# Optimization experiments

Measured on AMD Instinct MI355X. Metric: run time of the kernel, lower is better.

## Reference

```python
import jax, jax.numpy as jnp
import numpy as np

# Dims: batch=2, seqlen=L=384, d_inner=d=384, d_state=s=384, dt_rank=r=384, d_conv=4.
# NOTE: the original torch module only runs when L == d_inner == d_state == dt_rank
# (see its broadcasting in SelectiveScan and the Linear layer plumbing); we reproduce
# that exact (quirky) broadcast faithfully.
B_, L_, D_, S_, R_, K_ = 2, 384, 384, 384, 384, 4


def setup_inputs() -> dict:
    key = jax.random.key(0)
    ks = jax.random.split(key, 9)
    f32 = jnp.float32
    return {
        "x": jax.random.normal(ks[0], (B_, L_, D_), f32),
        "A_log": jax.random.normal(ks[1], (D_, S_), f32) * 0.02,
        "D": jax.random.normal(ks[2], (D_,), f32) * 0.02,
        "dt_w": jax.random.normal(ks[3], (D_, R_), f32) * 0.02,
        "dt_b": jax.random.normal(ks[4], (D_,), f32) * 0.02,
        "B_w": jax.random.normal(ks[5], (S_, D_), f32) * (1.0 / np.sqrt(D_)),
        "C_w": jax.random.normal(ks[6], (S_, D_), f32) * (1.0 / np.sqrt(D_)),
        "conv_w": jax.random.normal(ks[7], (D_, 1, K_), f32) * (1.0 / np.sqrt(K_)),
        "conv_b": jnp.zeros((D_,), f32),
    }


def _forward(x, A_log, D, dt_w, dt_b, B_w, C_w, conv_w, conv_b):
    b, L, d = x.shape
    A = -jnp.exp(A_log)                       # (d, s)
    dt = jax.nn.softplus(x @ dt_w.T + dt_b)   # (b, L, d)
    x_dbl = x @ B_w.T                         # (b, L, s)
    Bm = x_dbl @ B_w.T                        # (b, L, s)  (module applies B_proj twice)
    Cm = x_dbl @ C_w.T                        # (b, L, s)
    # causal depthwise conv1d: pad (k-1) on the left == torch pad k-1 then [:, :, :L]
    xc = jax.lax.conv_general_dilated(
        x.transpose(0, 2, 1), conv_w, (1,), [(conv_w.shape[-1] - 1, 0)],
        feature_group_count=d, dimension_numbers=("NCH", "OIH", "NCH"))
    xc = xc + conv_b[None, :, None]
    u = jax.nn.silu(xc.transpose(0, 2, 1))    # (b, L, d)
    # selective scan (faithful to the torch SelectiveScan broadcasting)
    deltaA = jnp.exp(dt[..., None] * A[None, None])          # (b, L, d, s)
    deltaB_u = dt[..., None] * Bm[:, None, :, :] * u[..., None]  # (b, L, d, s), needs L==d

    def step(h, inp):
        dA_i, dBu_i, C_i, u_i = inp
        h = dA_i * h + dBu_i                  # (b, d, s)
        y = jnp.sum(h * C_i[:, None, :], -1) + u_i * D  # (b, d)
        return h, y

    h0 = jnp.zeros((b, d, deltaA.shape[-1]), x.dtype)
    xs = (deltaA.transpose(1, 0, 2, 3), deltaB_u.transpose(1, 0, 2, 3),
          Cm.transpose(1, 0, 2), u.transpose(1, 0, 2))
    _, ys = jax.lax.scan(step, h0, xs)        # ys: (L, b, d)
    return ys.transpose(1, 0, 2)


def reference(x, A_log, D, dt_w, dt_b, B_w, C_w, conv_w, conv_b):
    return _forward(x, A_log, D, dt_w, dt_b, B_w, C_w, conv_w, conv_b)
```

## Files before the change

kernel.cpp:

```cpp
#include <hip/hip_runtime.h>
#include <math.h>

#define B_SZ 2
#define L_SZ 384
#define D_SZ 384
#define S_SZ 384
#define BLK_ELEMS (L_SZ * D_SZ)
#define TOT_ELEMS (B_SZ * L_SZ * D_SZ)
#define LOG2E 1.4426950408889634f

typedef __attribute__((ext_vector_type(8))) short bf16x8;
typedef __attribute__((ext_vector_type(4))) float f32x4;
typedef __attribute__((ext_vector_type(2))) unsigned int u32x2;

__device__ __forceinline__ float fexp2(float x) {
  return __builtin_amdgcn_exp2f(x);
}
__device__ __forceinline__ float softplus_f(float z) {
  return (z > 20.f) ? z : log1pf(__expf(z));
}
__device__ __forceinline__ unsigned short f2bf(float f) {
  unsigned int u = __float_as_uint(f);
  return (unsigned short)((u + 0x7FFFu + ((u >> 16) & 1u)) >> 16);
}
#define PIPELINE_FENCE() asm volatile("" ::: "memory")

template <int CTRL>
__device__ __forceinline__ float dpp_mov(float v) {
  return __int_as_float(
      __builtin_amdgcn_update_dpp(0, __float_as_int(v), CTRL, 0xF, 0xF, true));
}

__device__ __forceinline__ float fold_xor16(float r) {
#if __has_builtin(__builtin_amdgcn_permlane16_swap)
  const unsigned ru = __float_as_uint(r);
  u32x2 p = __builtin_amdgcn_permlane16_swap(ru, ru, false, false);
  return __uint_as_float(p[0]) + __uint_as_float(p[1]);
#else
  return r + __shfl_xor(r, 16, 64);
#endif
}
__device__ __forceinline__ float fold_xor32(float r) {
#if __has_builtin(__builtin_amdgcn_permlane32_swap)
  const unsigned ru = __float_as_uint(r);
  u32x2 p = __builtin_amdgcn_permlane32_swap(ru, ru, false, false);
  return __uint_as_float(p[0]) + __uint_as_float(p[1]);
#else
  return r + __shfl_xor(r, 32, 64);
#endif
}

__global__ __launch_bounds__(256) void cvt_bf16_kernel(
    const float* __restrict__ x, const float* __restrict__ dt_w,
    const float* __restrict__ B_w, const float* __restrict__ C_w,
    unsigned short* __restrict__ xbf, unsigned short* __restrict__ dtwbf,
    unsigned short* __restrict__ Bwbf, unsigned short* __restrict__ Cwbf) {
  const int blk = blockIdx.x;
  const float* src;
  unsigned short* dst;
  int base;
  if (blk < 288) { src = x; dst = xbf; base = blk; }
  else if (blk < 432) { src = dt_w; dst = dtwbf; base = blk - 288; }
  else if (blk < 576) { src = B_w; dst = Bwbf; base = blk - 432; }
  else { src = C_w; dst = Cwbf; base = blk - 576; }
  const int idx = base * 1024 + threadIdx.x * 4;
  const float4 v = *(const float4*)(src + idx);
  ushort4 o;
  o.x = f2bf(v.x); o.y = f2bf(v.y); o.z = f2bf(v.z); o.w = f2bf(v.w);
  *(ushort4*)(dst + idx) = o;
}

template <int MODE>
__global__ __launch_bounds__(128, 2) void mfma_dual_gemm(
    const unsigned short* __restrict__ Abf,
    const unsigned short* __restrict__ W1bf,
    const unsigned short* __restrict__ W2bf,
    const float* __restrict__ bias,
    float* __restrict__ O1, void* __restrict__ O2v) {
  __shared__ unsigned short sA[32 * 392];
  __shared__ unsigned short sW1[16 * 392];
  __shared__ unsigned short sW2[16 * 392];

  const int t = threadIdx.x;
  const int wv = t >> 6;
  const int lane = t & 63;
  const int nt = blockIdx.x;
  const int mrow = blockIdx.y;

  const unsigned short* Ab = Abf + mrow * 32 * 384;
  const unsigned short* W1b = W1bf + nt * 16 * 384;
  const unsigned short* W2b = W2bf + nt * 16 * 384;

#pragma unroll
  for (int it = 0; it < 12; ++it) {
    const int id = t + it * 128;
    const int row = id / 48, col = id - row * 48;
    *(bf16x8*)&sA[row * 392 + col * 8] = *(const bf16x8*)(Ab + id * 8);
  }
#pragma unroll
  for (int it = 0; it < 6; ++it) {
    const int id = t + it * 128;
    const int row = id / 48, col = id - row * 48;
    *(bf16x8*)&sW1[row * 392 + col * 8] = *(const bf16x8*)(W1b + id * 8);
    *(bf16x8*)&sW2[row * 392 + col * 8] = *(const bf16x8*)(W2b + id * 8);
  }
  __syncthreads();

  const int rc = lane & 15;
  const int quad = lane >> 4;
  bf16x8 af[12], w1f[12], w2f[12];
#pragma unroll
  for (int kt = 0; kt < 12; ++kt) {
    af[kt] = *(const bf16x8*)&sA[(wv * 16 + rc) * 392 + quad * 8 + kt * 32];
    w1f[kt] = *(const bf16x8*)&sW1[rc * 392 + quad * 8 + kt * 32];
    w2f[kt] = *(const bf16x8*)&sW2[rc * 392 + quad * 8 + kt * 32];
  }
  PIPELINE_FENCE();
  f32x4 acc1 = {0.f, 0.f, 0.f, 0.f};
  f32x4 acc2 = {0.f, 0.f, 0.f, 0.f};
#pragma unroll
  for (int kt = 0; kt < 12; ++kt) {
    acc1 = __builtin_amdgcn_mfma_f32_16x16x32_bf16(af[kt], w1f[kt], acc1, 0, 0, 0);
    acc2 = __builtin_amdgcn_mfma_f32_16x16x32_bf16(af[kt], w2f[kt], acc2, 0, 0, 0);
  }
  const int col = nt * 16 + rc;
  const int row0 = mrow * 32 + wv * 16 + quad * 4;
  if constexpr (MODE == 1) {
    unsigned short* O2 = (unsigned short*)O2v;
    const float bb = bias[col];
#pragma unroll
    for (int r = 0; r < 4; ++r) {
      O1[(row0 + r) * 384 + col] = softplus_f(acc1[r] + bb);
      O2[(row0 + r) * 384 + col] = f2bf(acc2[r]);
    }
  } else {
    float* O2 = (float*)O2v;
#pragma unroll
    for (int r = 0; r < 4; ++r) {
      O1[(row0 + r) * 384 + col] = acc1[r];
      O2[(row0 + r) * 384 + col] = acc2[r];
    }
  }
}

__global__ __launch_bounds__(256) void conv_tr_kernel(
    const float* __restrict__ x, const float* __restrict__ cw,
    const float* __restrict__ cb, const float* __restrict__ dt,
    float* __restrict__ u, float* __restrict__ dt_t,
    float* __restrict__ dtu_t) {
  __shared__ float Tdt[32][33];
  __shared__ float Tdu[32][33];
  const int tx = threadIdx.x;
  const int ty = threadIdx.y;
  const int b = blockIdx.z;
  const int i0 = blockIdx.y * 32;
  const int l0 = blockIdx.x * 32;
  const int gi = i0 + tx;
  const float cbv = cb[gi];
  const float cw0 = cw[gi * 4 + 0], cw1 = cw[gi * 4 + 1];
  const float cw2 = cw[gi * 4 + 2], cw3 = cw[gi * 4 + 3];
#pragma unroll
  for (int r = 0; r < 4; ++r) {
    const int l = l0 + ty + 8 * r;
    float acc = cbv;
    const float x3 = x[(b * L_SZ + l) * D_SZ + gi];
    const float x2 = (l >= 1) ? x[(b * L_SZ + l - 1) * D_SZ + gi] : 0.f;
    const float x1 = (l >= 2) ? x[(b * L_SZ + l - 2) * D_SZ + gi] : 0.f;
    const float x0 = (l >= 3) ? x[(b * L_SZ + l - 3) * D_SZ + gi] : 0.f;
    acc = fmaf(x0, cw0, acc);
    acc = fmaf(x1, cw1, acc);
    acc = fmaf(x2, cw2, acc);
    acc = fmaf(x3, cw3, acc);
    const float uv = acc / (1.f + __expf(-acc));
    const int off = (b * L_SZ + l) * D_SZ + gi;
    u[off] = uv;
    const float dtv = dt[off];
    Tdt[ty + 8 * r][tx] = dtv;
    Tdu[ty + 8 * r][tx] = dtv * uv;
  }
  __syncthreads();
#pragma unroll
  for (int r = 0; r < 4; ++r) {
    const int il = ty + 8 * r;
    const int off = (b * D_SZ + i0 + il) * L_SZ + l0 + tx;
    dt_t[off] = Tdt[tx][il];
    dtu_t[off] = Tdu[tx][il];
  }
}

struct ChunkS {
  f32x4 d0, d1, u0, u1;
  float c[8];
};

#define LOAD_CHUNK(K, B0, B1, B2, DTB, DUB)                                    \
  {                                                                            \
    asm volatile("global_load_dwordx4 %0, %1, off" : "=v"(K.d0) : "v"(DTB));   \
    asm volatile("global_load_dwordx4 %0, %1, off offset:16"                   \
                 : "=v"(K.d1) : "v"(DTB));                                     \
    asm volatile("global_load_dwordx4 %0, %1, off" : "=v"(K.u0) : "v"(DUB));   \
    asm volatile("global_load_dwordx4 %0, %1, off offset:16"                   \
                 : "=v"(K.u1) : "v"(DUB));                                     \
    asm volatile("global_load_dword %0, %1, off" : "=v"(K.c[0]) : "v"(B0));    \
    asm volatile("global_load_dword %0, %1, off offset:1536"                   \
                 : "=v"(K.c[1]) : "v"(B0));                                    \
    asm volatile("global_load_dword %0, %1, off offset:3072"                   \
                 : "=v"(K.c[2]) : "v"(B0));                                    \
    asm volatile("global_load_dword %0, %1, off" : "=v"(K.c[3]) : "v"(B1));    \
    asm volatile("global_load_dword %0, %1, off offset:1536"                   \
                 : "=v"(K.c[4]) : "v"(B1));                                    \
    asm volatile("global_load_dword %0, %1, off offset:3072"                   \
                 : "=v"(K.c[5]) : "v"(B1));                                    \
    asm volatile("global_load_dword %0, %1, off" : "=v"(K.c[6]) : "v"(B2));    \
    asm volatile("global_load_dword %0, %1, off offset:1536"                   \
                 : "=v"(K.c[7]) : "v"(B2));                                    \
  }

#define WAIT_CHUNK(K)                                                          \
  asm volatile("s_waitcnt vmcnt(24)"                                           \
               : "+v"(K.d0), "+v"(K.d1), "+v"(K.u0), "+v"(K.u1),               \
                 "+v"(K.c[0]), "+v"(K.c[1]), "+v"(K.c[2]), "+v"(K.c[3]),       \
                 "+v"(K.c[4]), "+v"(K.c[5]), "+v"(K.c[6]), "+v"(K.c[7]))

#define ADV_BASES()                                                            \
  { cb0 += 3072; cb1 += 3072; cb2 += 3072; dtB += 8; duB += 8; }

__global__ __launch_bounds__(384, 4) void scan_kernel(
    const float* __restrict__ A_log, const float* __restrict__ dt_t,
    const float* __restrict__ dtu_t, const float* __restrict__ Bm,
    const float* __restrict__ Cm, float* __restrict__ part) {
  const int bid = blockIdx.x;
  const int xcd = bid & 7;
  const int sid = xcd * 96 + (bid >> 3);
  const int w = threadIdx.x >> 6;
  const int lane = threadIdx.x & 63;
  const int b = sid / D_SZ;
  const int i = sid % D_SZ;
  const int j = w * 64 + lane;

  const float a2 = -__expf(A_log[i * S_SZ + j]) * LOG2E;
  const float bw = Bm[(b * D_SZ + i) * S_SZ + j];
  float h = 0.f;

  const float* dtB = dt_t + (b * D_SZ + i) * L_SZ;
  const float* duB = dtu_t + (b * D_SZ + i) * L_SZ;
  const float* cmrow = Cm + b * BLK_ELEMS + j;
  const float* cb0 = cmrow;
  const float* cb1 = cmrow + 3 * D_SZ;
  const float* cb2 = cmrow + 6 * D_SZ;

  const int sq = (((lane >> 3) & 1) << 2) | (((lane >> 2) & 1) << 1) | (lane & 1);
  const bool storer = (lane & 0x32) == 0;
  float* pstore = part + ((w * B_SZ + b) * D_SZ + i) * L_SZ + sq;

  asm volatile("" :: "v"(a2), "v"(bw));
  asm volatile("s_waitcnt vmcnt(0)");

  auto compute_chunk = [&](ChunkS& K) {
    float acc[8];
    const float dts[8] = {K.d0[0], K.d0[1], K.d0[2], K.d0[3],
                          K.d1[0], K.d1[1], K.d1[2], K.d1[3]};
    const float dus[8] = {K.u0[0], K.u0[1], K.u0[2], K.u0[3],
                          K.u1[0], K.u1[1], K.u1[2], K.u1[3]};
#pragma unroll
    for (int s = 0; s < 8; ++s) {
      const float e = fexp2(dts[s] * a2);
      h = fmaf(e, h, bw * dus[s]);
      acc[s] = h * K.c[s];
    }
    {
      const bool hi = (lane & 8) != 0;
#pragma unroll
      for (int q = 0; q < 4; ++q) {
        const float keep = hi ? acc[q + 4] : acc[q];
        const float send = hi ? acc[q] : acc[q + 4];
        acc[q] = keep + dpp_mov<0x140>(send);
      }
    }
    {
      const bool hi = (lane & 4) != 0;
#pragma unroll
      for (int q = 0; q < 2; ++q) {
        const float keep = hi ? acc[q + 2] : acc[q];
        const float send = hi ? acc[q] : acc[q + 2];
        acc[q] = keep + dpp_mov<0x141>(send);
      }
    }
    {
      const bool hi = (lane & 1) != 0;
      const float keep = hi ? acc[1] : acc[0];
      const float send = hi ? acc[0] : acc[1];
      acc[0] = keep + dpp_mov<0xB1>(send);
    }
    float r = acc[0];
    r += dpp_mov<0x4E>(r);
    r = fold_xor16(r);
    r = fold_xor32(r);
    if (storer) *pstore = r;
    pstore += 8;
  };

  ChunkS K0, K1, K2;
  LOAD_CHUNK(K0, cb0, cb1, cb2, dtB, duB);
  ADV_BASES();
  LOAD_CHUNK(K1, cb0, cb1, cb2, dtB, duB);
  ADV_BASES();
#pragma unroll 1
  for (int it = 0; it < 16; ++it) {
    LOAD_CHUNK(K2, cb0, cb1, cb2, dtB, duB);
    ADV_BASES();
    WAIT_CHUNK(K0);
    compute_chunk(K0);
    LOAD_CHUNK(K0, cb0, cb1, cb2, dtB, duB);
    ADV_BASES();
    WAIT_CHUNK(K1);
    compute_chunk(K1);
    LOAD_CHUNK(K1, cb0, cb1, cb2, dtB, duB);
    ADV_BASES();
    WAIT_CHUNK(K2);
    compute_chunk(K2);
  }
}

__global__ __launch_bounds__(256) void combine_kernel(
    const float* __restrict__ part, const float* __restrict__ u,
    const float* __restrict__ Dv, float* __restrict__ y) {
  __shared__ float T[32][33];
  const int tx = threadIdx.x;
  const int ty0 = threadIdx.y;
  const int b = blockIdx.z;
  const int i0 = blockIdx.y * 32;
  const int l0 = blockIdx.x * 32;
#pragma unroll
  for (int r = 0; r < 4; ++r) {
    const int il = ty0 + 8 * r;
    float s = 0.f;
#pragma unroll
    for (int w = 0; w < 6; ++w)
      s += part[((w * B_SZ + b) * D_SZ + i0 + il) * L_SZ + l0 + tx];
    T[il][tx] = s;
  }
  __syncthreads();
#pragma unroll
  for (int r = 0; r < 4; ++r) {
    const int ll = ty0 + 8 * r;
    const int gi = i0 + tx;
    const int off = (b * L_SZ + l0 + ll) * D_SZ + gi;
    y[off] = fmaf(u[off], Dv[gi], T[tx][ll]);
  }
}

extern "C" void kernel_launch(void* const* d_in, const int* in_sizes, int n_in,
                              void* d_out, int out_size, void* d_ws,
                              size_t ws_size, hipStream_t stream) {
  const float* x = (const float*)d_in[0];
  const float* A_log = (const float*)d_in[1];
  const float* D = (const float*)d_in[2];
  const float* dt_w = (const float*)d_in[3];
  const float* dt_b = (const float*)d_in[4];
  const float* B_w = (const float*)d_in[5];
  const float* C_w = (const float*)d_in[6];
  const float* conv_w = (const float*)d_in[7];
  const float* conv_b = (const float*)d_in[8];
  float* y = (float*)d_out;

  float* ws = (float*)d_ws;
  float* dt = ws;
  float* u = ws + TOT_ELEMS;
  float* Bm = ws + 2 * TOT_ELEMS;
  float* Cm = ws + 3 * TOT_ELEMS;
  float* dt_t = ws + 4 * TOT_ELEMS;
  float* dtu_t = ws + 5 * TOT_ELEMS;
  float* part = ws + 6 * TOT_ELEMS;
  unsigned short* bfarea = (unsigned short*)(ws + 12 * TOT_ELEMS);
  unsigned short* xbf = bfarea;
  unsigned short* dtwbf = bfarea + 294912;
  unsigned short* Bwbf = bfarea + 442368;
  unsigned short* Cwbf = bfarea + 589824;
  unsigned short* xdblbf = bfarea + 737280;

  cvt_bf16_kernel<<<720, 256, 0, stream>>>(x, dt_w, B_w, C_w, xbf, dtwbf, Bwbf, Cwbf);
  mfma_dual_gemm<1><<<dim3(24, 24), 128, 0, stream>>>(xbf, dtwbf, Bwbf, dt_b, dt, xdblbf);
  mfma_dual_gemm<2><<<dim3(24, 24), 128, 0, stream>>>(xdblbf, Bwbf, Cwbf, nullptr, Bm, Cm);
  conv_tr_kernel<<<dim3(L_SZ / 32, D_SZ / 32, B_SZ), dim3(32, 8), 0, stream>>>(
      x, conv_w, conv_b, dt, u, dt_t, dtu_t);
  scan_kernel<<<768, 384, 0, stream>>>(A_log, dt_t, dtu_t, Bm, Cm, part);
  combine_kernel<<<dim3(L_SZ / 32, D_SZ / 32, B_SZ), dim3(32, 8), 0, stream>>>(
      part, u, D, y);
}
```

Before: 139.7 us.

## Fuse bf16 conversion into GEMM loads, transpose Cm, split scan into wave blocks

Removes the separate fp32-to-bf16 conversion kernel: the GEMMs now load fp32 inputs and weights and convert them in-register with packed bf16 conversion instructions while filling LDS. The conv/transpose kernel additionally writes a transposed copy of Cm, so each scan lane can read contiguous dwordx4 vectors instead of eight strided scalar loads per chunk. The scan launch changes from 768 blocks of 384 threads to 4608 single-wave blocks. The trade-offs are an extra transpose write and read of Cm, and weights being converted redundantly in every GEMM block.

```diff
diff --git a/kernel.cpp b/kernel.cpp
--- a/kernel.cpp
+++ b/kernel.cpp
@@ -24,6 +24,17 @@
   return (unsigned short)((u + 0x7FFFu + ((u >> 16) & 1u)) >> 16);
 }
 #define PIPELINE_FENCE() asm volatile("" ::: "memory")
+
+__device__ __forceinline__ bf16x8 cvt8(const float* p) {
+  const f32x4 v0 = *(const f32x4*)p;
+  const f32x4 v1 = *(const f32x4*)(p + 4);
+  union { unsigned int u[4]; bf16x8 v; } r;
+  asm("v_cvt_pk_bf16_f32 %0, %1, %2" : "=v"(r.u[0]) : "v"(v0[0]), "v"(v0[1]));
+  asm("v_cvt_pk_bf16_f32 %0, %1, %2" : "=v"(r.u[1]) : "v"(v0[2]), "v"(v0[3]));
+  asm("v_cvt_pk_bf16_f32 %0, %1, %2" : "=v"(r.u[2]) : "v"(v1[0]), "v"(v1[1]));
+  asm("v_cvt_pk_bf16_f32 %0, %1, %2" : "=v"(r.u[3]) : "v"(v1[2]), "v"(v1[3]));
+  return r.v;
+}
 
 template <int CTRL>
 __device__ __forceinline__ float dpp_mov(float v) {
@@ -50,32 +61,10 @@
 #endif
 }
 
-__global__ __launch_bounds__(256) void cvt_bf16_kernel(
-    const float* __restrict__ x, const float* __restrict__ dt_w,
-    const float* __restrict__ B_w, const float* __restrict__ C_w,
-    unsigned short* __restrict__ xbf, unsigned short* __restrict__ dtwbf,
-    unsigned short* __restrict__ Bwbf, unsigned short* __restrict__ Cwbf) {
-  const int blk = blockIdx.x;
-  const float* src;
-  unsigned short* dst;
-  int base;
-  if (blk < 288) { src = x; dst = xbf; base = blk; }
-  else if (blk < 432) { src = dt_w; dst = dtwbf; base = blk - 288; }
-  else if (blk < 576) { src = B_w; dst = Bwbf; base = blk - 432; }
-  else { src = C_w; dst = Cwbf; base = blk - 576; }
-  const int idx = base * 1024 + threadIdx.x * 4;
-  const float4 v = *(const float4*)(src + idx);
-  ushort4 o;
-  o.x = f2bf(v.x); o.y = f2bf(v.y); o.z = f2bf(v.z); o.w = f2bf(v.w);
-  *(ushort4*)(dst + idx) = o;
-}
-
 template <int MODE>
 __global__ __launch_bounds__(128, 2) void mfma_dual_gemm(
-    const unsigned short* __restrict__ Abf,
-    const unsigned short* __restrict__ W1bf,
-    const unsigned short* __restrict__ W2bf,
-    const float* __restrict__ bias,
+    const void* __restrict__ Av, const float* __restrict__ W1,
+    const float* __restrict__ W2, const float* __restrict__ bias,
     float* __restrict__ O1, void* __restrict__ O2v) {
   __shared__ unsigned short sA[32 * 392];
   __shared__ unsigned short sW1[16 * 392];
@@ -87,22 +76,32 @@
   const int nt = blockIdx.x;
   const int mrow = blockIdx.y;
 
-  const unsigned short* Ab = Abf + mrow * 32 * 384;
-  const unsigned short* W1b = W1bf + nt * 16 * 384;
-  const unsigned short* W2b = W2bf + nt * 16 * 384;
-
-#pragma unroll
-  for (int it = 0; it < 12; ++it) {
-    const int id = t + it * 128;
-    const int row = id / 48, col = id - row * 48;
-    *(bf16x8*)&sA[row * 392 + col * 8] = *(const bf16x8*)(Ab + id * 8);
+  const float* W1b = W1 + nt * 16 * 384;
+  const float* W2b = W2 + nt * 16 * 384;
+
+  if constexpr (MODE == 1) {
+    const float* Ab = (const float*)Av + mrow * 32 * 384;
+#pragma unroll
+    for (int it = 0; it < 12; ++it) {
+      const int id = t + it * 128;
+      const int row = id / 48, col = id - row * 48;
+      *(bf16x8*)&sA[row * 392 + col * 8] = cvt8(Ab + id * 8);
+    }
+  } else {
+    const unsigned short* Ab = (const unsigned short*)Av + mrow * 32 * 384;
+#pragma unroll
+    for (int it = 0; it < 12; ++it) {
+      const int id = t + it * 128;
+      const int row = id / 48, col = id - row * 48;
+      *(bf16x8*)&sA[row * 392 + col * 8] = *(const bf16x8*)(Ab + id * 8);
+    }
   }
 #pragma unroll
   for (int it = 0; it < 6; ++it) {
     const int id = t + it * 128;
     const int row = id / 48, col = id - row * 48;
-    *(bf16x8*)&sW1[row * 392 + col * 8] = *(const bf16x8*)(W1b + id * 8);
-    *(bf16x8*)&sW2[row * 392 + col * 8] = *(const bf16x8*)(W2b + id * 8);
+    *(bf16x8*)&sW1[row * 392 + col * 8] = cvt8(W1b + id * 8);
+    *(bf16x8*)&sW2[row * 392 + col * 8] = cvt8(W2b + id * 8);
   }
   __syncthreads();
 
@@ -146,10 +145,12 @@
 __global__ __launch_bounds__(256) void conv_tr_kernel(
     const float* __restrict__ x, const float* __restrict__ cw,
     const float* __restrict__ cb, const float* __restrict__ dt,
+    const float* __restrict__ Cmi,
     float* __restrict__ u, float* __restrict__ dt_t,
-    float* __restrict__ dtu_t) {
+    float* __restrict__ dtu_t, float* __restrict__ Cm_t) {
   __shared__ float Tdt[32][33];
   __shared__ float Tdu[32][33];
+  __shared__ float Tcm[32][33];
   const int tx = threadIdx.x;
   const int ty = threadIdx.y;
   const int b = blockIdx.z;
@@ -177,6 +178,7 @@
     const float dtv = dt[off];
     Tdt[ty + 8 * r][tx] = dtv;
     Tdu[ty + 8 * r][tx] = dtv * uv;
+    Tcm[ty + 8 * r][tx] = Cmi[off];
   }
   __syncthreads();
 #pragma unroll
@@ -185,15 +187,15 @@
     const int off = (b * D_SZ + i0 + il) * L_SZ + l0 + tx;
     dt_t[off] = Tdt[tx][il];
     dtu_t[off] = Tdu[tx][il];
+    Cm_t[off] = Tcm[tx][il];
   }
 }
 
 struct ChunkS {
-  f32x4 d0, d1, u0, u1;
-  float c[8];
+  f32x4 d0, d1, u0, u1, c0, c1;
 };
 
-#define LOAD_CHUNK(K, B0, B1, B2, DTB, DUB)                                    \
+#define LOAD_CHUNK(K, CMT, DTB, DUB)                                           \
   {                                                                            \
     asm volatile("global_load_dwordx4 %0, %1, off" : "=v"(K.d0) : "v"(DTB));   \
     asm volatile("global_load_dwordx4 %0, %1, off offset:16"                   \
@@ -201,39 +203,29 @@
     asm volatile("global_load_dwordx4 %0, %1, off" : "=v"(K.u0) : "v"(DUB));   \
     asm volatile("global_load_dwordx4 %0, %1, off offset:16"                   \
                  : "=v"(K.u1) : "v"(DUB));                                     \
-    asm volatile("global_load_dword %0, %1, off" : "=v"(K.c[0]) : "v"(B0));    \
-    asm volatile("global_load_dword %0, %1, off offset:1536"                   \
-                 : "=v"(K.c[1]) : "v"(B0));                                    \
-    asm volatile("global_load_dword %0, %1, off offset:3072"                   \
-                 : "=v"(K.c[2]) : "v"(B0));                                    \
-    asm volatile("global_load_dword %0, %1, off" : "=v"(K.c[3]) : "v"(B1));    \
-    asm volatile("global_load_dword %0, %1, off offset:1536"                   \
-                 : "=v"(K.c[4]) : "v"(B1));                                    \
-    asm volatile("global_load_dword %0, %1, off offset:3072"                   \
-                 : "=v"(K.c[5]) : "v"(B1));                                    \
-    asm volatile("global_load_dword %0, %1, off" : "=v"(K.c[6]) : "v"(B2));    \
-    asm volatile("global_load_dword %0, %1, off offset:1536"                   \
-                 : "=v"(K.c[7]) : "v"(B2));                                    \
+    asm volatile("global_load_dwordx4 %0, %1, off" : "=v"(K.c0) : "v"(CMT));   \
+    asm volatile("global_load_dwordx4 %0, %1, off offset:16"                   \
+                 : "=v"(K.c1) : "v"(CMT));                                     \
   }
 
 #define WAIT_CHUNK(K)                                                          \
-  asm volatile("s_waitcnt vmcnt(24)"                                           \
+  asm volatile("s_waitcnt vmcnt(12)"                                           \
                : "+v"(K.d0), "+v"(K.d1), "+v"(K.u0), "+v"(K.u1),               \
-                 "+v"(K.c[0]), "+v"(K.c[1]), "+v"(K.c[2]), "+v"(K.c[3]),       \
-                 "+v"(K.c[4]), "+v"(K.c[5]), "+v"(K.c[6]), "+v"(K.c[7]))
+                 "+v"(K.c0), "+v"(K.c1))
 
 #define ADV_BASES()                                                            \
-  { cb0 += 3072; cb1 += 3072; cb2 += 3072; dtB += 8; duB += 8; }
-
-__global__ __launch_bounds__(384, 4) void scan_kernel(
+  { cmt += 8; dtB += 8; duB += 8; }
+
+__global__ __launch_bounds__(64, 4) void scan_kernel(
     const float* __restrict__ A_log, const float* __restrict__ dt_t,
     const float* __restrict__ dtu_t, const float* __restrict__ Bm,
-    const float* __restrict__ Cm, float* __restrict__ part) {
+    const float* __restrict__ Cm_t, float* __restrict__ part) {
   const int bid = blockIdx.x;
   const int xcd = bid & 7;
-  const int sid = xcd * 96 + (bid >> 3);
-  const int w = threadIdx.x >> 6;
-  const int lane = threadIdx.x & 63;
+  const int slot = bid >> 3;
+  const int sid = xcd * 96 + slot / 6;
+  const int w = slot % 6;
+  const int lane = threadIdx.x;
   const int b = sid / D_SZ;
   const int i = sid % D_SZ;
   const int j = w * 64 + lane;
@@ -244,10 +236,7 @@
 
   const float* dtB = dt_t + (b * D_SZ + i) * L_SZ;
   const float* duB = dtu_t + (b * D_SZ + i) * L_SZ;
-  const float* cmrow = Cm + b * BLK_ELEMS + j;
-  const float* cb0 = cmrow;
-  const float* cb1 = cmrow + 3 * D_SZ;
-  const float* cb2 = cmrow + 6 * D_SZ;
+  const float* cmt = Cm_t + (b * S_SZ + j) * L_SZ;
 
   const int sq = (((lane >> 3) & 1) << 2) | (((lane >> 2) & 1) << 1) | (lane & 1);
   const bool storer = (lane & 0x32) == 0;
@@ -262,11 +251,13 @@
                           K.d1[0], K.d1[1], K.d1[2], K.d1[3]};
     const float dus[8] = {K.u0[0], K.u0[1], K.u0[2], K.u0[3],
                           K.u1[0], K.u1[1], K.u1[2], K.u1[3]};
+    const float cs[8] = {K.c0[0], K.c0[1], K.c0[2], K.c0[3],
+                         K.c1[0], K.c1[1], K.c1[2], K.c1[3]};
 #pragma unroll
     for (int s = 0; s < 8; ++s) {
       const float e = fexp2(dts[s] * a2);
       h = fmaf(e, h, bw * dus[s]);
-      acc[s] = h * K.c[s];
+      acc[s] = h * cs[s];
     }
     {
       const bool hi = (lane & 8) != 0;
@@ -301,21 +292,21 @@
   };
 
   ChunkS K0, K1, K2;
-  LOAD_CHUNK(K0, cb0, cb1, cb2, dtB, duB);
+  LOAD_CHUNK(K0, cmt, dtB, duB);
   ADV_BASES();
-  LOAD_CHUNK(K1, cb0, cb1, cb2, dtB, duB);
+  LOAD_CHUNK(K1, cmt, dtB, duB);
   ADV_BASES();
 #pragma unroll 1
   for (int it = 0; it < 16; ++it) {
-    LOAD_CHUNK(K2, cb0, cb1, cb2, dtB, duB);
+    LOAD_CHUNK(K2, cmt, dtB, duB);
     ADV_BASES();
     WAIT_CHUNK(K0);
     compute_chunk(K0);
-    LOAD_CHUNK(K0, cb0, cb1, cb2, dtB, duB);
+    LOAD_CHUNK(K0, cmt, dtB, duB);
     ADV_BASES();
     WAIT_CHUNK(K1);
     compute_chunk(K1);
-    LOAD_CHUNK(K1, cb0, cb1, cb2, dtB, duB);
+    LOAD_CHUNK(K1, cmt, dtB, duB);
     ADV_BASES();
     WAIT_CHUNK(K2);
     compute_chunk(K2);
@@ -372,19 +363,14 @@
   float* dt_t = ws + 4 * TOT_ELEMS;
   float* dtu_t = ws + 5 * TOT_ELEMS;
   float* part = ws + 6 * TOT_ELEMS;
-  unsigned short* bfarea = (unsigned short*)(ws + 12 * TOT_ELEMS);
-  unsigned short* xbf = bfarea;
-  unsigned short* dtwbf = bfarea + 294912;
-  unsigned short* Bwbf = bfarea + 442368;
-  unsigned short* Cwbf = bfarea + 589824;
-  unsigned short* xdblbf = bfarea + 737280;
-
-  cvt_bf16_kernel<<<720, 256, 0, stream>>>(x, dt_w, B_w, C_w, xbf, dtwbf, Bwbf, Cwbf);
-  mfma_dual_gemm<1><<<dim3(24, 24), 128, 0, stream>>>(xbf, dtwbf, Bwbf, dt_b, dt, xdblbf);
-  mfma_dual_gemm<2><<<dim3(24, 24), 128, 0, stream>>>(xdblbf, Bwbf, Cwbf, nullptr, Bm, Cm);
+  float* Cm_t = ws + 12 * TOT_ELEMS;
+  unsigned short* xdblbf = (unsigned short*)(ws + 13 * TOT_ELEMS);
+
+  mfma_dual_gemm<1><<<dim3(24, 24), 128, 0, stream>>>(x, dt_w, B_w, dt_b, dt, xdblbf);
+  mfma_dual_gemm<2><<<dim3(24, 24), 128, 0, stream>>>(xdblbf, B_w, C_w, nullptr, Bm, Cm);
   conv_tr_kernel<<<dim3(L_SZ / 32, D_SZ / 32, B_SZ), dim3(32, 8), 0, stream>>>(
-      x, conv_w, conv_b, dt, u, dt_t, dtu_t);
-  scan_kernel<<<768, 384, 0, stream>>>(A_log, dt_t, dtu_t, Bm, Cm, part);
+      x, conv_w, conv_b, dt, Cm, u, dt_t, dtu_t, Cm_t);
+  scan_kernel<<<4608, 64, 0, stream>>>(A_log, dt_t, dtu_t, Bm, Cm_t, part);
   combine_kernel<<<dim3(L_SZ / 32, D_SZ / 32, B_SZ), dim3(32, 8), 0, stream>>>(
       part, u, D, y);
 }
```

After: 172.3 us. 23.3% more time.

## Fuse bf16 conversion into GEMM loads and combine step into scan kernel

Applied to the files above, without the earlier changes.

Drops the separate fp32-to-bf16 conversion kernel: the GEMMs now read fp32 inputs and weights directly and pack them to bf16 with v_cvt_pk_bf16_f32 while staging into shared memory. The scan kernel now writes its per-wave partial sums to LDS, reduces the six waves itself and writes y with the u*D term, which removes the global partial buffer and the combine kernel launch. The scan loop is peeled so the final chunks are not followed by out-of-range prefetches. In exchange the weights are converted redundantly in each GEMM block, and the final y stores stride by D, so they are uncoalesced.

```diff
diff --git a/kernel.cpp b/kernel.cpp
--- a/kernel.cpp
+++ b/kernel.cpp
@@ -24,6 +24,17 @@
   return (unsigned short)((u + 0x7FFFu + ((u >> 16) & 1u)) >> 16);
 }
 #define PIPELINE_FENCE() asm volatile("" ::: "memory")
+
+__device__ __forceinline__ bf16x8 cvt8(const float* p) {
+  const f32x4 v0 = *(const f32x4*)p;
+  const f32x4 v1 = *(const f32x4*)(p + 4);
+  union { unsigned int u[4]; bf16x8 v; } r;
+  asm("v_cvt_pk_bf16_f32 %0, %1, %2" : "=v"(r.u[0]) : "v"(v0[0]), "v"(v0[1]));
+  asm("v_cvt_pk_bf16_f32 %0, %1, %2" : "=v"(r.u[1]) : "v"(v0[2]), "v"(v0[3]));
+  asm("v_cvt_pk_bf16_f32 %0, %1, %2" : "=v"(r.u[2]) : "v"(v1[0]), "v"(v1[1]));
+  asm("v_cvt_pk_bf16_f32 %0, %1, %2" : "=v"(r.u[3]) : "v"(v1[2]), "v"(v1[3]));
+  return r.v;
+}
 
 template <int CTRL>
 __device__ __forceinline__ float dpp_mov(float v) {
@@ -50,32 +61,10 @@
 #endif
 }
 
-__global__ __launch_bounds__(256) void cvt_bf16_kernel(
-    const float* __restrict__ x, const float* __restrict__ dt_w,
-    const float* __restrict__ B_w, const float* __restrict__ C_w,
-    unsigned short* __restrict__ xbf, unsigned short* __restrict__ dtwbf,
-    unsigned short* __restrict__ Bwbf, unsigned short* __restrict__ Cwbf) {
-  const int blk = blockIdx.x;
-  const float* src;
-  unsigned short* dst;
-  int base;
-  if (blk < 288) { src = x; dst = xbf; base = blk; }
-  else if (blk < 432) { src = dt_w; dst = dtwbf; base = blk - 288; }
-  else if (blk < 576) { src = B_w; dst = Bwbf; base = blk - 432; }
-  else { src = C_w; dst = Cwbf; base = blk - 576; }
-  const int idx = base * 1024 + threadIdx.x * 4;
-  const float4 v = *(const float4*)(src + idx);
-  ushort4 o;
-  o.x = f2bf(v.x); o.y = f2bf(v.y); o.z = f2bf(v.z); o.w = f2bf(v.w);
-  *(ushort4*)(dst + idx) = o;
-}
-
 template <int MODE>
 __global__ __launch_bounds__(128, 2) void mfma_dual_gemm(
-    const unsigned short* __restrict__ Abf,
-    const unsigned short* __restrict__ W1bf,
-    const unsigned short* __restrict__ W2bf,
-    const float* __restrict__ bias,
+    const void* __restrict__ Av, const float* __restrict__ W1,
+    const float* __restrict__ W2, const float* __restrict__ bias,
     float* __restrict__ O1, void* __restrict__ O2v) {
   __shared__ unsigned short sA[32 * 392];
   __shared__ unsigned short sW1[16 * 392];
@@ -87,22 +76,32 @@
   const int nt = blockIdx.x;
   const int mrow = blockIdx.y;
 
-  const unsigned short* Ab = Abf + mrow * 32 * 384;
-  const unsigned short* W1b = W1bf + nt * 16 * 384;
-  const unsigned short* W2b = W2bf + nt * 16 * 384;
-
-#pragma unroll
-  for (int it = 0; it < 12; ++it) {
-    const int id = t + it * 128;
-    const int row = id / 48, col = id - row * 48;
-    *(bf16x8*)&sA[row * 392 + col * 8] = *(const bf16x8*)(Ab + id * 8);
+  const float* W1b = W1 + nt * 16 * 384;
+  const float* W2b = W2 + nt * 16 * 384;
+
+  if constexpr (MODE == 1) {
+    const float* Ab = (const float*)Av + mrow * 32 * 384;
+#pragma unroll
+    for (int it = 0; it < 12; ++it) {
+      const int id = t + it * 128;
+      const int row = id / 48, col = id - row * 48;
+      *(bf16x8*)&sA[row * 392 + col * 8] = cvt8(Ab + id * 8);
+    }
+  } else {
+    const unsigned short* Ab = (const unsigned short*)Av + mrow * 32 * 384;
+#pragma unroll
+    for (int it = 0; it < 12; ++it) {
+      const int id = t + it * 128;
+      const int row = id / 48, col = id - row * 48;
+      *(bf16x8*)&sA[row * 392 + col * 8] = *(const bf16x8*)(Ab + id * 8);
+    }
   }
 #pragma unroll
   for (int it = 0; it < 6; ++it) {
     const int id = t + it * 128;
     const int row = id / 48, col = id - row * 48;
-    *(bf16x8*)&sW1[row * 392 + col * 8] = *(const bf16x8*)(W1b + id * 8);
-    *(bf16x8*)&sW2[row * 392 + col * 8] = *(const bf16x8*)(W2b + id * 8);
+    *(bf16x8*)&sW1[row * 392 + col * 8] = cvt8(W1b + id * 8);
+    *(bf16x8*)&sW2[row * 392 + col * 8] = cvt8(W2b + id * 8);
   }
   __syncthreads();
 
@@ -216,8 +215,8 @@
                  : "=v"(K.c[7]) : "v"(B2));                                    \
   }
 
-#define WAIT_CHUNK(K)                                                          \
-  asm volatile("s_waitcnt vmcnt(24)"                                           \
+#define WAIT_CHUNK_IMM(K, S)                                                   \
+  asm volatile("s_waitcnt vmcnt(" S ")"                                        \
                : "+v"(K.d0), "+v"(K.d1), "+v"(K.u0), "+v"(K.u1),               \
                  "+v"(K.c[0]), "+v"(K.c[1]), "+v"(K.c[2]), "+v"(K.c[3]),       \
                  "+v"(K.c[4]), "+v"(K.c[5]), "+v"(K.c[6]), "+v"(K.c[7]))
@@ -228,7 +227,9 @@
 __global__ __launch_bounds__(384, 4) void scan_kernel(
     const float* __restrict__ A_log, const float* __restrict__ dt_t,
     const float* __restrict__ dtu_t, const float* __restrict__ Bm,
-    const float* __restrict__ Cm, float* __restrict__ part) {
+    const float* __restrict__ Cm, const float* __restrict__ u,
+    const float* __restrict__ Dv, float* __restrict__ y) {
+  __shared__ float sP[6 * L_SZ];
   const int bid = blockIdx.x;
   const int xcd = bid & 7;
   const int sid = xcd * 96 + (bid >> 3);
@@ -251,7 +252,7 @@
 
   const int sq = (((lane >> 3) & 1) << 2) | (((lane >> 2) & 1) << 1) | (lane & 1);
   const bool storer = (lane & 0x32) == 0;
-  float* pstore = part + ((w * B_SZ + b) * D_SZ + i) * L_SZ + sq;
+  int pidx = w * L_SZ + sq;
 
   asm volatile("" :: "v"(a2), "v"(bw));
   asm volatile("s_waitcnt vmcnt(0)");
@@ -296,8 +297,8 @@
     r += dpp_mov<0x4E>(r);
     r = fold_xor16(r);
     r = fold_xor32(r);
-    if (storer) *pstore = r;
-    pstore += 8;
+    if (storer) sP[pidx] = r;
+    pidx += 8;
   };
 
   ChunkS K0, K1, K2;
@@ -306,48 +307,34 @@
   LOAD_CHUNK(K1, cb0, cb1, cb2, dtB, duB);
   ADV_BASES();
 #pragma unroll 1
-  for (int it = 0; it < 16; ++it) {
+  for (int it = 0; it < 15; ++it) {
     LOAD_CHUNK(K2, cb0, cb1, cb2, dtB, duB);
     ADV_BASES();
-    WAIT_CHUNK(K0);
+    WAIT_CHUNK_IMM(K0, "24");
     compute_chunk(K0);
     LOAD_CHUNK(K0, cb0, cb1, cb2, dtB, duB);
     ADV_BASES();
-    WAIT_CHUNK(K1);
+    WAIT_CHUNK_IMM(K1, "24");
     compute_chunk(K1);
     LOAD_CHUNK(K1, cb0, cb1, cb2, dtB, duB);
     ADV_BASES();
-    WAIT_CHUNK(K2);
+    WAIT_CHUNK_IMM(K2, "24");
     compute_chunk(K2);
   }
-}
-
-__global__ __launch_bounds__(256) void combine_kernel(
-    const float* __restrict__ part, const float* __restrict__ u,
-    const float* __restrict__ Dv, float* __restrict__ y) {
-  __shared__ float T[32][33];
-  const int tx = threadIdx.x;
-  const int ty0 = threadIdx.y;
-  const int b = blockIdx.z;
-  const int i0 = blockIdx.y * 32;
-  const int l0 = blockIdx.x * 32;
-#pragma unroll
-  for (int r = 0; r < 4; ++r) {
-    const int il = ty0 + 8 * r;
-    float s = 0.f;
-#pragma unroll
-    for (int w = 0; w < 6; ++w)
-      s += part[((w * B_SZ + b) * D_SZ + i0 + il) * L_SZ + l0 + tx];
-    T[il][tx] = s;
-  }
+  LOAD_CHUNK(K2, cb0, cb1, cb2, dtB, duB);
+  WAIT_CHUNK_IMM(K0, "24");
+  compute_chunk(K0);
+  WAIT_CHUNK_IMM(K1, "12");
+  compute_chunk(K1);
+  WAIT_CHUNK_IMM(K2, "0");
+  compute_chunk(K2);
+
   __syncthreads();
-#pragma unroll
-  for (int r = 0; r < 4; ++r) {
-    const int ll = ty0 + 8 * r;
-    const int gi = i0 + tx;
-    const int off = (b * L_SZ + l0 + ll) * D_SZ + gi;
-    y[off] = fmaf(u[off], Dv[gi], T[tx][ll]);
-  }
+  const int l = threadIdx.x;
+  const float s6 = sP[l] + sP[L_SZ + l] + sP[2 * L_SZ + l] +
+                   sP[3 * L_SZ + l] + sP[4 * L_SZ + l] + sP[5 * L_SZ + l];
+  const int off = (b * L_SZ + l) * D_SZ + i;
+  y[off] = fmaf(u[off], Dv[i], s6);
 }
 
 extern "C" void kernel_launch(void* const* d_in, const int* in_sizes, int n_in,
@@ -371,20 +358,11 @@
   float* Cm = ws + 3 * TOT_ELEMS;
   float* dt_t = ws + 4 * TOT_ELEMS;
   float* dtu_t = ws + 5 * TOT_ELEMS;
-  float* part = ws + 6 * TOT_ELEMS;
-  unsigned short* bfarea = (unsigned short*)(ws + 12 * TOT_ELEMS);
-  unsigned short* xbf = bfarea;
-  unsigned short* dtwbf = bfarea + 294912;
-  unsigned short* Bwbf = bfarea + 442368;
-  unsigned short* Cwbf = bfarea + 589824;
-  unsigned short* xdblbf = bfarea + 737280;
-
-  cvt_bf16_kernel<<<720, 256, 0, stream>>>(x, dt_w, B_w, C_w, xbf, dtwbf, Bwbf, Cwbf);
-  mfma_dual_gemm<1><<<dim3(24, 24), 128, 0, stream>>>(xbf, dtwbf, Bwbf, dt_b, dt, xdblbf);
-  mfma_dual_gemm<2><<<dim3(24, 24), 128, 0, stream>>>(xdblbf, Bwbf, Cwbf, nullptr, Bm, Cm);
+  unsigned short* xdblbf = (unsigned short*)(ws + 6 * TOT_ELEMS);
+
+  mfma_dual_gemm<1><<<dim3(24, 24), 128, 0, stream>>>(x, dt_w, B_w, dt_b, dt, xdblbf);
+  mfma_dual_gemm<2><<<dim3(24, 24), 128, 0, stream>>>(xdblbf, B_w, C_w, nullptr, Bm, Cm);
   conv_tr_kernel<<<dim3(L_SZ / 32, D_SZ / 32, B_SZ), dim3(32, 8), 0, stream>>>(
       x, conv_w, conv_b, dt, u, dt_t, dtu_t);
-  scan_kernel<<<768, 384, 0, stream>>>(A_log, dt_t, dtu_t, Bm, Cm, part);
-  combine_kernel<<<dim3(L_SZ / 32, D_SZ / 32, B_SZ), dim3(32, 8), 0, stream>>>(
-      part, u, D, y);
-}
+  scan_kernel<<<768, 384, 0, stream>>>(A_log, dt_t, dtu_t, Bm, Cm, u, D, y);
+}
```

Measured after the change: 145.3 us. 1.04x slower.
